# Kernel tuning notes

Hardware: AMD Instinct MI355X
Metric: run time of the kernel (lower is better)

The kernel has to match this reference:

```python
import jax, jax.numpy as jnp
import numpy as np

B, S, NX, H = 4, 1024, 1024, 16
D = NX // H  # 64 head dim
NEG = -1e9


def setup_inputs() -> dict:
    key = jax.random.key(0)
    k1, k2, k3 = jax.random.split(key, 3)
    x = jax.random.normal(k1, (B, S, NX), dtype=jnp.float32)
    # boolean mask, True = masked (causal: cannot attend to future)
    causal = ~jnp.tril(jnp.ones((S, S), dtype=bool))
    mask_self_attention = causal[None, None, :, :]  # [1,1,S,S]
    w_attn = jax.random.normal(k2, (NX, 3 * NX), dtype=jnp.float32) * 0.02
    b_attn = jnp.zeros((3 * NX,), dtype=jnp.float32)
    w_proj = jax.random.normal(k3, (NX, NX), dtype=jnp.float32) * 0.02
    b_proj = jnp.zeros((NX,), dtype=jnp.float32)
    return {"x": x, "mask_self_attention": mask_self_attention,
            "w_attn": w_attn, "b_attn": b_attn,
            "w_proj": w_proj, "b_proj": b_proj}


def reference(x, mask_self_attention, w_attn, b_attn, w_proj, b_proj):
    # c_attn: fused QKV projection
    qkv = jnp.einsum('bsn,nm->bsm', x, w_attn) + b_attn  # [B,S,3*NX]
    q, k, v = jnp.split(qkv, 3, axis=-1)
    # split heads -> [B,H,S,D]
    def heads(t):
        return t.reshape(B, S, H, D).transpose(0, 2, 1, 3)
    q, k, v = heads(q), heads(k), heads(v)
    # present = stack(key [B,H,S,D], value [B,H,S,D]) -> [2,B,H,S,D]
    present = jnp.stack((k, v))
    # scaled dot-product attention with boolean mask (True = masked)
    w = jnp.einsum('bhqd,bhkd->bhqk', q, k) / jnp.sqrt(jnp.float32(D))
    w = jnp.where(mask_self_attention, NEG, w)
    w = jax.nn.softmax(w, axis=-1)
    # attn_pdrop is identity in eval mode
    a = jnp.einsum('bhqk,bhkd->bhqd', w, v)
    # merge heads -> [B,S,NX]
    a = a.transpose(0, 2, 1, 3).reshape(B, S, NX)
    # c_proj
    a = jnp.einsum('bsn,nm->bsm', a, w_proj) + b_proj
    return (a, present)
```

## Files before the change

kernel.cpp:

```cpp
#include <hip/hip_runtime.h>
#include <math.h>
#include <stdint.h>

#define BATCH 4
#define SEQ   1024
#define NXDIM 1024
#define NHEAD 16
#define DHEAD 64
#define QKVN  3072
#define MROWS 4096
#define KDIM  1024

typedef short short8 __attribute__((ext_vector_type(8)));
typedef float f32x4  __attribute__((ext_vector_type(4)));

typedef const __attribute__((address_space(1))) unsigned int* gptr_t;
typedef __attribute__((address_space(3))) unsigned int* lptr_t;

__device__ __forceinline__ unsigned short f2bf(float f) {
    unsigned int u = __float_as_uint(f);
    u += 0x7FFF + ((u >> 16) & 1);
    return (unsigned short)(u >> 16);
}
__device__ __forceinline__ float bf2f(unsigned short h) {
    return __uint_as_float(((unsigned int)h) << 16);
}
__device__ __forceinline__ unsigned pk_hi_rtne(float a, float b) {
    unsigned ua = __float_as_uint(a), ub = __float_as_uint(b);
    ua += 0x7FFF + ((ua >> 16) & 1);
    ub += 0x7FFF + ((ub >> 16) & 1);
    return __builtin_amdgcn_perm(ub, ua, 0x07060302u);
}
__device__ __forceinline__ unsigned pk_hi_trunc(float a, float b) {
    return __builtin_amdgcn_perm(__float_as_uint(b), __float_as_uint(a), 0x07060302u);
}
__device__ __forceinline__ float trunc_bf(float a) {
    return __uint_as_float(__float_as_uint(a) & 0xFFFF0000u);
}
__device__ __forceinline__ float rtne_bf(float a) {
    unsigned u = __float_as_uint(a);
    u += 0x7FFF + ((u >> 16) & 1);
    return __uint_as_float(u & 0xFFFF0000u);
}

__global__ __launch_bounds__(256) void split_x_kernel(
    const float* __restrict__ x, unsigned short* __restrict__ xh,
    unsigned short* __restrict__ xl)
{
    const int t = blockIdx.x * 256 + threadIdx.x;
    const int tile = t >> 9, u = t & 511;
    const int mt = tile >> 5, kt = tile & 31;
    const int g = u >> 6, khalf = (u >> 4) & 3, r16 = u & 15;
    const int m = mt * 128 + g * 16 + r16;
    const int k = kt * 32 + khalf * 8;
    const float4 v0 = *(const float4*)&x[(size_t)m * KDIM + k];
    const float4 v1 = *(const float4*)&x[(size_t)m * KDIM + k + 4];
    const float vv[8] = {v0.x, v0.y, v0.z, v0.w, v1.x, v1.y, v1.z, v1.w};
    unsigned short h[8], l[8];
    #pragma unroll
    for (int e = 0; e < 8; ++e) {
        h[e] = f2bf(vv[e]);
        l[e] = f2bf(vv[e] - bf2f(h[e]));
    }
    uint4 ph, pl;
    ph.x = (unsigned)h[0] | ((unsigned)h[1] << 16);
    ph.y = (unsigned)h[2] | ((unsigned)h[3] << 16);
    ph.z = (unsigned)h[4] | ((unsigned)h[5] << 16);
    ph.w = (unsigned)h[6] | ((unsigned)h[7] << 16);
    pl.x = (unsigned)l[0] | ((unsigned)l[1] << 16);
    pl.y = (unsigned)l[2] | ((unsigned)l[3] << 16);
    pl.z = (unsigned)l[4] | ((unsigned)l[5] << 16);
    pl.w = (unsigned)l[6] | ((unsigned)l[7] << 16);
    *(uint4*)&xh[(size_t)t * 8] = ph;
    *(uint4*)&xl[(size_t)t * 8] = pl;
}

__global__ __launch_bounds__(256) void split_w_kernel(
    const float* __restrict__ w, unsigned short* __restrict__ wh,
    unsigned short* __restrict__ wl, int N)
{
    const int t = blockIdx.x * 256 + threadIdx.x;
    const int tile = t >> 9, u = t & 511;
    const int nt = tile >> 5, kt = tile & 31;
    const int gn = u >> 6, khalf = (u >> 4) & 3, c16 = u & 15;
    const int n = nt * 128 + gn * 16 + c16;
    const int k0 = kt * 32 + khalf * 8;
    unsigned short h[8], l[8];
    #pragma unroll
    for (int e = 0; e < 8; ++e) {
        const float v = w[(size_t)(k0 + e) * N + n];
        h[e] = f2bf(v);
        l[e] = f2bf(v - bf2f(h[e]));
    }
    uint4 ph, pl;
    ph.x = (unsigned)h[0] | ((unsigned)h[1] << 16);
    ph.y = (unsigned)h[2] | ((unsigned)h[3] << 16);
    ph.z = (unsigned)h[4] | ((unsigned)h[5] << 16);
    ph.w = (unsigned)h[6] | ((unsigned)h[7] << 16);
    pl.x = (unsigned)l[0] | ((unsigned)l[1] << 16);
    pl.y = (unsigned)l[2] | ((unsigned)l[3] << 16);
    pl.z = (unsigned)l[4] | ((unsigned)l[5] << 16);
    pl.w = (unsigned)l[6] | ((unsigned)l[7] << 16);
    *(uint4*)&wh[(size_t)t * 8] = ph;
    *(uint4*)&wl[(size_t)t * 8] = pl;
}

template<int EPI>
__global__ __launch_bounds__(256, 2) void mfma_gemm_kernel(
    const unsigned short* __restrict__ Ahg, const unsigned short* __restrict__ Alg,
    const unsigned short* __restrict__ Bhg, const unsigned short* __restrict__ Blg,
    const float* __restrict__ bias,
    float* __restrict__ o0, float* __restrict__ o1, float* __restrict__ o2,
    unsigned short* __restrict__ qh_o, unsigned short* __restrict__ ql_o)
{
    __shared__ unsigned char lds[32768];
    const int tid = threadIdx.x;
    const int wave = tid >> 6, lane = tid & 63;
    const int bm = blockIdx.y, bn = blockIdx.x;

    const unsigned short* mysrc;
    if      (wave == 0) mysrc = Ahg + (size_t)bm * 32 * 4096;
    else if (wave == 1) mysrc = Alg + (size_t)bm * 32 * 4096;
    else if (wave == 2) mysrc = Bhg + (size_t)bn * 32 * 4096;
    else                mysrc = Blg + (size_t)bn * 32 * 4096;

    const f32x4 fzero = {0.f, 0.f, 0.f, 0.f};
    f32x4 acc[4][4];
    #pragma unroll
    for (int i = 0; i < 4; ++i)
        #pragma unroll
        for (int j = 0; j < 4; ++j) acc[i][j] = fzero;

    const int frag_off = ((lane >> 4) << 8) + ((lane & 15) << 4);
    const int ag = (wave >> 1) * 4;
    const int bg = (wave & 1) * 4;

    for (int kt = 0; kt < 32; ++kt) {
        __syncthreads();
        const unsigned short* src = mysrc + kt * 4096;
        #pragma unroll
        for (int c = 0; c < 8; ++c) {
            const unsigned short* gsrc = src + (c << 9) + (lane << 3);
            __builtin_amdgcn_global_load_lds(
                (gptr_t)(uintptr_t)gsrc,
                (lptr_t)(uintptr_t)(&lds[(wave << 13) + (c << 10)]),
                16, 0, 0);
        }
        __syncthreads();

        short8 ah[4], al[4], bh[4], bl[4];
        #pragma unroll
        for (int i = 0; i < 4; ++i) {
            const int ao = (ag + i) * 1024 + frag_off;
            const int bo = (bg + i) * 1024 + frag_off;
            ah[i] = __builtin_bit_cast(short8, *(const uint4*)&lds[ao]);
            al[i] = __builtin_bit_cast(short8, *(const uint4*)&lds[8192 + ao]);
            bh[i] = __builtin_bit_cast(short8, *(const uint4*)&lds[16384 + bo]);
            bl[i] = __builtin_bit_cast(short8, *(const uint4*)&lds[24576 + bo]);
        }
        #pragma unroll
        for (int i = 0; i < 4; ++i)
            #pragma unroll
            for (int j = 0; j < 4; ++j) {
                acc[i][j] = __builtin_amdgcn_mfma_f32_16x16x32_bf16(ah[i], bh[j], acc[i][j], 0, 0, 0);
                acc[i][j] = __builtin_amdgcn_mfma_f32_16x16x32_bf16(ah[i], bl[j], acc[i][j], 0, 0, 0);
                acc[i][j] = __builtin_amdgcn_mfma_f32_16x16x32_bf16(al[i], bh[j], acc[i][j], 0, 0, 0);
            }
    }

    const int gm_base = bm * 128 + (wave >> 1) * 64 + ((lane >> 4) << 2);
    const int gn_base = bn * 128 + (wave & 1) * 64 + (lane & 15);
    #pragma unroll
    for (int j = 0; j < 4; ++j) {
        const int gn = gn_base + j * 16;
        const float bj = bias[gn];
        if (EPI == 0) {
            #pragma unroll
            for (int i = 0; i < 4; ++i)
                #pragma unroll
                for (int r = 0; r < 4; ++r)
                    o0[(size_t)(gm_base + i * 16 + r) * NXDIM + gn] = acc[i][j][r] + bj;
        } else {
            const int sec = gn >> 10;
            const int hh  = (gn >> 6) & 15;
            const int d   = gn & 63;
            #pragma unroll
            for (int i = 0; i < 4; ++i)
                #pragma unroll
                for (int r = 0; r < 4; ++r) {
                    const int gm = gm_base + i * 16 + r;
                    const int bq = gm >> 10, s = gm & 1023;
                    const size_t idx = (((size_t)bq * NHEAD + hh) * SEQ + s) * DHEAD + d;
                    const float val = acc[i][j][r] + bj;
                    if (sec == 1)      o1[idx] = val;
                    else if (sec == 2) o2[idx] = val;
                    else {
                        const float vq = val * 0.18033688f;
                        const unsigned short hq = f2bf(vq);
                        qh_o[idx] = hq;
                        ql_o[idx] = f2bf(vq - bf2f(hq));
                    }
                }
        }
    }
}

__global__ __launch_bounds__(256, 3) void attn_kernel(
    const unsigned short* __restrict__ qh_g, const unsigned short* __restrict__ ql_g,
    const float* __restrict__ kbuf, const float* __restrict__ vbuf,
    unsigned short* __restrict__ ahi, unsigned short* __restrict__ alo)
{
    __shared__ unsigned char lds[49152];
    unsigned char* const Kh  = lds;
    unsigned char* const Kl  = lds + 8192;
    unsigned char* const Vth = lds + 16384;
    unsigned char* const Vtl = lds + 24576;

    const int tid  = threadIdx.x;
    const int wave = tid >> 6, lane = tid & 63;
    const int l15  = lane & 15, lg = lane >> 4;
    const int pp = (int)(blockIdx.x & 7);
    const int bh = (int)(blockIdx.x >> 3);
    unsigned char* const Ps = lds + 32768 + (wave << 12);

    const float* kb = kbuf + (size_t)bh * SEQ * DHEAD;
    const float* vb = vbuf + (size_t)bh * SEQ * DHEAD;

    const int krow = tid >> 2, kdq = (tid & 3) << 4;
    const int vrow = tid & 63, vkq = tid >> 6;

    float4 kreg[4];
    float  vreg[16];

    auto load_tile = [&](int kb0) {
        #pragma unroll
        for (int c = 0; c < 4; ++c)
            kreg[c] = *(const float4*)&kb[(size_t)(kb0 + krow) * DHEAD + kdq + 4 * c];
        #pragma unroll
        for (int kk = 0; kk < 16; ++kk)
            vreg[kk] = vb[(size_t)(kb0 + vkq * 16 + kk) * DHEAD + vrow];
    };
    auto commit = [&]() {
        #pragma unroll
        for (int c = 0; c < 4; ++c) {
            const float4 f = kreg[c];
            const unsigned h01 = pk_hi_rtne(f.x, f.y);
            const unsigned h23 = pk_hi_rtne(f.z, f.w);
            const unsigned l01 = pk_hi_trunc(f.x - rtne_bf(f.x), f.y - rtne_bf(f.y));
            const unsigned l23 = pk_hi_trunc(f.z - rtne_bf(f.z), f.w - rtne_bf(f.w));
            const int slot = ((tid & 3) << 1) + (c >> 1);
            const int addr = krow * 128 + ((slot ^ (krow & 7)) << 4) + ((c & 1) << 3);
            *(uint2*)(Kh + addr) = make_uint2(h01, h23);
            *(uint2*)(Kl + addr) = make_uint2(l01, l23);
        }
        unsigned vhp[8], vlp[8];
        #pragma unroll
        for (int p = 0; p < 8; ++p) {
            const float a = vreg[2 * p], b2 = vreg[2 * p + 1];
            vhp[p] = pk_hi_trunc(a, b2);
            vlp[p] = pk_hi_trunc(a - trunc_bf(a), b2 - trunc_bf(b2));
        }
        const int vs0 = vkq << 1;
        const int vb0 = vrow * 128;
        const int vsw = vrow & 7;
        *(uint4*)(Vth + vb0 + (((vs0    ) ^ vsw) << 4)) = make_uint4(vhp[0], vhp[1], vhp[2], vhp[3]);
        *(uint4*)(Vth + vb0 + (((vs0 + 1) ^ vsw) << 4)) = make_uint4(vhp[4], vhp[5], vhp[6], vhp[7]);
        *(uint4*)(Vtl + vb0 + (((vs0    ) ^ vsw) << 4)) = make_uint4(vlp[0], vlp[1], vlp[2], vlp[3]);
        *(uint4*)(Vtl + vb0 + (((vs0 + 1) ^ vsw) << 4)) = make_uint4(vlp[4], vlp[5], vlp[6], vlp[7]);
    };

    const int fsw = lg ^ (l15 & 7);
    const int hh = bh & 15, bq = bh >> 4;

    short8 vone;
    #pragma unroll
    for (int e = 0; e < 8; ++e) vone[e] = (short)0x3F80;

    auto process = [&](int q0, int nt, bool has_next) {
        short8 qhf[2], qlf[2];
        {
            const size_t qb0 = ((size_t)bh * SEQ + q0 + wave * 16 + l15) * DHEAD + lg * 8;
            qhf[0] = *(const short8*)(qh_g + qb0);
            qhf[1] = *(const short8*)(qh_g + qb0 + 32);
            qlf[0] = *(const short8*)(ql_g + qb0);
            qlf[1] = *(const short8*)(ql_g + qb0 + 32);
        }
        float mprev[4];
        f32x4 lacc = (f32x4){0.f, 0.f, 0.f, 0.f};
        f32x4 oacc[4];
        #pragma unroll
        for (int r = 0; r < 4; ++r) mprev[r] = -3.0e38f;
        #pragma unroll
        for (int jd = 0; jd < 4; ++jd) oacc[jd] = (f32x4){0.f, 0.f, 0.f, 0.f};

        for (int kt = 0; kt < nt; ++kt) {
            __syncthreads();
            const bool pf = (kt + 1 < nt) || has_next;
            if (pf) load_tile((kt + 1 < nt) ? (kt + 1) << 6 : 0);

            f32x4 sacc[4];
            #pragma unroll
            for (int j = 0; j < 4; ++j) sacc[j] = (f32x4){0.f, 0.f, 0.f, 0.f};
            __builtin_amdgcn_s_setprio(1);
            #pragma unroll
            for (int ks = 0; ks < 2; ++ks) {
                #pragma unroll
                for (int j = 0; j < 4; ++j) {
                    const int addr = ((j << 4) + l15) * 128 + ((fsw ^ (ks << 2)) << 4);
                    const short8 khf = *(const short8*)(Kh + addr);
                    const short8 klf = *(const short8*)(Kl + addr);
                    sacc[j] = __builtin_amdgcn_mfma_f32_16x16x32_bf16(qhf[ks], khf, sacc[j], 0, 0, 0);
                    sacc[j] = __builtin_amdgcn_mfma_f32_16x16x32_bf16(qhf[ks], klf, sacc[j], 0, 0, 0);
                    sacc[j] = __builtin_amdgcn_mfma_f32_16x16x32_bf16(qlf[ks], khf, sacc[j], 0, 0, 0);
                }
            }
            __builtin_amdgcn_s_setprio(0);

            const int k0 = kt << 6;
            const bool diag = (k0 == q0);
            float mx[4];
            #pragma unroll
            for (int r = 0; r < 4; ++r) {
                const int qg = q0 + wave * 16 + lg * 4 + r;
                float m_ = -3.0e38f;
                #pragma unroll
                for (int j = 0; j < 4; ++j) {
                    float sv = sacc[j][r];
                    if (diag && (k0 + (j << 4) + l15) > qg) sv = -1.0e9f;
                    sacc[j][r] = sv;
                    m_ = fmaxf(m_, sv);
                }
                m_ = fmaxf(m_, __shfl_xor(m_, 1));
                m_ = fmaxf(m_, __shfl_xor(m_, 2));
                m_ = fmaxf(m_, __shfl_xor(m_, 4));
                m_ = fmaxf(m_, __shfl_xor(m_, 8));
                mx[r] = m_;
            }

            bool need = false;
            #pragma unroll
            for (int r = 0; r < 4; ++r) need |= (mx[r] > mprev[r] + 8.0f);
            if (__any(need)) {
                #pragma unroll
                for (int r = 0; r < 4; ++r) {
                    const float mnew = fmaxf(mprev[r], mx[r]);
                    const float corr = exp2f(mprev[r] - mnew);
                    lacc[r] *= corr;
                    #pragma unroll
                    for (int jd = 0; jd < 4; ++jd) oacc[jd][r] *= corr;
                    mprev[r] = mnew;
                }
            }

            #pragma unroll
            for (int j = 0; j < 4; ++j)
                #pragma unroll
                for (int r = 0; r < 4; ++r) {
                    const float p = exp2f(sacc[j][r] - mprev[r]);
                    const unsigned up = __float_as_uint(p);
                    const float plo = p - __uint_as_float(up & 0xFFFF0000u);
                    const unsigned packed = (up & 0xFFFF0000u) | (__float_as_uint(plo) >> 16);
                    const int qq = lg * 4 + r;
                    const int kcol = (j << 4) + l15;
                    const int addr = qq * 256 + (((kcol >> 2) ^ qq) << 4) + ((kcol & 3) << 2);
                    *(unsigned*)(Ps + addr) = packed;
                }

            __builtin_amdgcn_s_setprio(1);
            #pragma unroll
            for (int ks = 0; ks < 2; ++ks) {
                const int s0 = (ks << 3) + (lg << 1);
                const uint4 pk0 = *(const uint4*)(Ps + l15 * 256 + (((s0    ) ^ l15) << 4));
                const uint4 pk1 = *(const uint4*)(Ps + l15 * 256 + (((s0 + 1) ^ l15) << 4));
                uint4 uh, ul;
                uh.x = __builtin_amdgcn_perm(pk0.y, pk0.x, 0x07060302u);
                uh.y = __builtin_amdgcn_perm(pk0.w, pk0.z, 0x07060302u);
                uh.z = __builtin_amdgcn_perm(pk1.y, pk1.x, 0x07060302u);
                uh.w = __builtin_amdgcn_perm(pk1.w, pk1.z, 0x07060302u);
                ul.x = __builtin_amdgcn_perm(pk0.y, pk0.x, 0x05040100u);
                ul.y = __builtin_amdgcn_perm(pk0.w, pk0.z, 0x05040100u);
                ul.z = __builtin_amdgcn_perm(pk1.y, pk1.x, 0x05040100u);
                ul.w = __builtin_amdgcn_perm(pk1.w, pk1.z, 0x05040100u);
                const short8 phf = __builtin_bit_cast(short8, uh);
                const short8 plf = __builtin_bit_cast(short8, ul);
                lacc = __builtin_amdgcn_mfma_f32_16x16x32_bf16(phf, vone, lacc, 0, 0, 0);
                lacc = __builtin_amdgcn_mfma_f32_16x16x32_bf16(plf, vone, lacc, 0, 0, 0);
                #pragma unroll
                for (int jd = 0; jd < 4; ++jd) {
                    const int vaddr = ((jd << 4) + l15) * 128 + ((fsw ^ (ks << 2)) << 4);
                    const short8 vhf = *(const short8*)(Vth + vaddr);
                    const short8 vlf = *(const short8*)(Vtl + vaddr);
                    oacc[jd] = __builtin_amdgcn_mfma_f32_16x16x32_bf16(phf, vhf, oacc[jd], 0, 0, 0);
                    oacc[jd] = __builtin_amdgcn_mfma_f32_16x16x32_bf16(phf, vlf, oacc[jd], 0, 0, 0);
                    oacc[jd] = __builtin_amdgcn_mfma_f32_16x16x32_bf16(plf, vhf, oacc[jd], 0, 0, 0);
                }
            }
            __builtin_amdgcn_s_setprio(0);

            __syncthreads();
            if (pf) commit();
        }

        float inv[4];
        #pragma unroll
        for (int r = 0; r < 4; ++r) inv[r] = 1.0f / lacc[r];
        #pragma unroll
        for (int jd = 0; jd < 4; ++jd) {
            const int kcol = (hh << 6) + (jd << 4) + l15;
            const int ktile = kcol >> 5, khalf = (kcol & 31) >> 3, k7 = kcol & 7;
            #pragma unroll
            for (int r = 0; r < 4; ++r) {
                const int m = (bq << 10) + q0 + wave * 16 + lg * 4 + r;
                const float o = oacc[jd][r] * inv[r];
                const unsigned short hv = f2bf(o);
                const unsigned short lv = f2bf(o - bf2f(hv));
                const size_t off = ((size_t)((m >> 7) * 32 + ktile) << 12)
                                 + (size_t)((((m & 127) >> 4) << 9) + (khalf << 7) + ((m & 15) << 3) + k7);
                ahi[off] = hv;
                alo[off] = lv;
            }
        }
    };

    load_tile(0);
    commit();
    process(pp << 6, pp + 1, true);
    process((15 - pp) << 6, 16 - pp, false);
}

extern "C" void kernel_launch(void* const* d_in, const int* in_sizes, int n_in,
                              void* d_out, int out_size, void* d_ws, size_t ws_size,
                              hipStream_t stream) {
    const float* x      = (const float*)d_in[0];
    const float* w_attn = (const float*)d_in[2];
    const float* b_attn = (const float*)d_in[3];
    const float* w_proj = (const float*)d_in[4];
    const float* b_proj = (const float*)d_in[5];

    float* out = (float*)d_out;
    float* kbuf = out + (size_t)BATCH * SEQ * NXDIM;
    float* vbuf = kbuf + (size_t)BATCH * NHEAD * SEQ * DHEAD;
    unsigned short* qh = (unsigned short*)out;
    unsigned short* ql = qh + (size_t)BATCH * NHEAD * SEQ * DHEAD;

    unsigned char* ws = (unsigned char*)d_ws;
    unsigned short* xh  = (unsigned short*)(ws);
    unsigned short* xl  = (unsigned short*)(ws + (8u  << 20));
    unsigned short* wah = (unsigned short*)(ws + (16u << 20));
    unsigned short* wal = (unsigned short*)(ws + (22u << 20));
    unsigned short* wph = (unsigned short*)(ws + (28u << 20));
    unsigned short* wpl = (unsigned short*)(ws + (30u << 20));
    unsigned short* ah  = xh;
    unsigned short* al  = xl;

    split_x_kernel<<<2048, 256, 0, stream>>>(x, xh, xl);
    split_w_kernel<<<1536, 256, 0, stream>>>(w_attn, wah, wal, QKVN);
    split_w_kernel<<<512,  256, 0, stream>>>(w_proj, wpl == nullptr ? nullptr : wph, wpl, NXDIM);
    mfma_gemm_kernel<1><<<dim3(24, 32), 256, 0, stream>>>(
        xh, xl, wah, wal, b_attn, nullptr, kbuf, vbuf, qh, ql);
    attn_kernel<<<512, 256, 0, stream>>>(qh, ql, kbuf, vbuf, ah, al);
    mfma_gemm_kernel<0><<<dim3(8, 32), 256, 0, stream>>>(
        ah, al, wph, wpl, b_proj, out, nullptr, nullptr, nullptr, nullptr);
}
```

Measured before the change: 273.5 us.

## Double-buffer GEMM LDS staging and merge the three split kernels into one launch

The GEMM kernel now uses two 32 KB LDS buffers, prefetching the next K tile via global_load_lds while the current tile feeds MFMA. This replaces one of the two barriers per iteration and aims to overlap memory latency with compute. Separately, the x and weight bf16 hi/lo split kernels are fused into a single launch with block-range dispatch to cut launch overhead. The larger 64 KB LDS footprint may reduce how many blocks fit per CU compared with the launch bound of 2, and there is no explicit wait on the async LDS loads before the barrier, which relies on __syncthreads draining them.

```diff
diff --git a/kernel.cpp b/kernel.cpp
--- a/kernel.cpp
+++ b/kernel.cpp
@@ -43,19 +43,9 @@
     return __uint_as_float(u & 0xFFFF0000u);
 }
 
-__global__ __launch_bounds__(256) void split_x_kernel(
-    const float* __restrict__ x, unsigned short* __restrict__ xh,
-    unsigned short* __restrict__ xl)
+__device__ __forceinline__ void split_store8(
+    const float* vv, unsigned short* dh, unsigned short* dl, size_t t)
 {
-    const int t = blockIdx.x * 256 + threadIdx.x;
-    const int tile = t >> 9, u = t & 511;
-    const int mt = tile >> 5, kt = tile & 31;
-    const int g = u >> 6, khalf = (u >> 4) & 3, r16 = u & 15;
-    const int m = mt * 128 + g * 16 + r16;
-    const int k = kt * 32 + khalf * 8;
-    const float4 v0 = *(const float4*)&x[(size_t)m * KDIM + k];
-    const float4 v1 = *(const float4*)&x[(size_t)m * KDIM + k + 4];
-    const float vv[8] = {v0.x, v0.y, v0.z, v0.w, v1.x, v1.y, v1.z, v1.w};
     unsigned short h[8], l[8];
     #pragma unroll
     for (int e = 0; e < 8; ++e) {
@@ -71,38 +61,45 @@
     pl.y = (unsigned)l[2] | ((unsigned)l[3] << 16);
     pl.z = (unsigned)l[4] | ((unsigned)l[5] << 16);
     pl.w = (unsigned)l[6] | ((unsigned)l[7] << 16);
-    *(uint4*)&xh[(size_t)t * 8] = ph;
-    *(uint4*)&xl[(size_t)t * 8] = pl;
-}
-
-__global__ __launch_bounds__(256) void split_w_kernel(
-    const float* __restrict__ w, unsigned short* __restrict__ wh,
-    unsigned short* __restrict__ wl, int N)
+    *(uint4*)&dh[t * 8] = ph;
+    *(uint4*)&dl[t * 8] = pl;
+}
+
+__global__ __launch_bounds__(256) void split_all_kernel(
+    const float* __restrict__ x, const float* __restrict__ w_attn,
+    const float* __restrict__ w_proj,
+    unsigned short* __restrict__ xh, unsigned short* __restrict__ xl,
+    unsigned short* __restrict__ wah, unsigned short* __restrict__ wal,
+    unsigned short* __restrict__ wph, unsigned short* __restrict__ wpl)
 {
-    const int t = blockIdx.x * 256 + threadIdx.x;
-    const int tile = t >> 9, u = t & 511;
-    const int nt = tile >> 5, kt = tile & 31;
-    const int gn = u >> 6, khalf = (u >> 4) & 3, c16 = u & 15;
-    const int n = nt * 128 + gn * 16 + c16;
-    const int k0 = kt * 32 + khalf * 8;
-    unsigned short h[8], l[8];
-    #pragma unroll
-    for (int e = 0; e < 8; ++e) {
-        const float v = w[(size_t)(k0 + e) * N + n];
-        h[e] = f2bf(v);
-        l[e] = f2bf(v - bf2f(h[e]));
+    const int blk = blockIdx.x;
+    if (blk < 2048) {
+        const int t = blk * 256 + threadIdx.x;
+        const int tile = t >> 9, u = t & 511;
+        const int mt = tile >> 5, kt = tile & 31;
+        const int g = u >> 6, khalf = (u >> 4) & 3, r16 = u & 15;
+        const int m = mt * 128 + g * 16 + r16;
+        const int k = kt * 32 + khalf * 8;
+        const float4 v0 = *(const float4*)&x[(size_t)m * KDIM + k];
+        const float4 v1 = *(const float4*)&x[(size_t)m * KDIM + k + 4];
+        const float vv[8] = {v0.x, v0.y, v0.z, v0.w, v1.x, v1.y, v1.z, v1.w};
+        split_store8(vv, xh, xl, (size_t)t);
+    } else {
+        const float* w;
+        unsigned short *dh, *dl;
+        int t, N;
+        if (blk < 3584) { w = w_attn; dh = wah; dl = wal; N = QKVN;  t = (blk - 2048) * 256 + threadIdx.x; }
+        else            { w = w_proj; dh = wph; dl = wpl; N = NXDIM; t = (blk - 3584) * 256 + threadIdx.x; }
+        const int tile = t >> 9, u = t & 511;
+        const int nt = tile >> 5, kt = tile & 31;
+        const int gn = u >> 6, khalf = (u >> 4) & 3, c16 = u & 15;
+        const int n = nt * 128 + gn * 16 + c16;
+        const int k0 = kt * 32 + khalf * 8;
+        float vv[8];
+        #pragma unroll
+        for (int e = 0; e < 8; ++e) vv[e] = w[(size_t)(k0 + e) * N + n];
+        split_store8(vv, dh, dl, (size_t)t);
     }
-    uint4 ph, pl;
-    ph.x = (unsigned)h[0] | ((unsigned)h[1] << 16);
-    ph.y = (unsigned)h[2] | ((unsigned)h[3] << 16);
-    ph.z = (unsigned)h[4] | ((unsigned)h[5] << 16);
-    ph.w = (unsigned)h[6] | ((unsigned)h[7] << 16);
-    pl.x = (unsigned)l[0] | ((unsigned)l[1] << 16);
-    pl.y = (unsigned)l[2] | ((unsigned)l[3] << 16);
-    pl.z = (unsigned)l[4] | ((unsigned)l[5] << 16);
-    pl.w = (unsigned)l[6] | ((unsigned)l[7] << 16);
-    *(uint4*)&wh[(size_t)t * 8] = ph;
-    *(uint4*)&wl[(size_t)t * 8] = pl;
 }
 
 template<int EPI>
@@ -113,7 +110,7 @@
     float* __restrict__ o0, float* __restrict__ o1, float* __restrict__ o2,
     unsigned short* __restrict__ qh_o, unsigned short* __restrict__ ql_o)
 {
-    __shared__ unsigned char lds[32768];
+    __shared__ unsigned char lds[65536];
     const int tid = threadIdx.x;
     const int wave = tid >> 6, lane = tid & 63;
     const int bm = blockIdx.y, bn = blockIdx.x;
@@ -134,29 +131,36 @@
     const int frag_off = ((lane >> 4) << 8) + ((lane & 15) << 4);
     const int ag = (wave >> 1) * 4;
     const int bg = (wave & 1) * 4;
-
+    const int wq = wave << 13;
+
+    auto stage = [&](int buf, int kt) {
+        const unsigned short* src = mysrc + kt * 4096;
+        #pragma unroll
+        for (int c = 0; c < 8; ++c) {
+            __builtin_amdgcn_global_load_lds(
+                (gptr_t)(uintptr_t)(src + (c << 9) + (lane << 3)),
+                (lptr_t)(uintptr_t)(&lds[(buf << 15) + wq + (c << 10)]),
+                16, 0, 0);
+        }
+    };
+
+    stage(0, 0);
+    __syncthreads();
+
+    int cur = 0;
     for (int kt = 0; kt < 32; ++kt) {
-        __syncthreads();
-        const unsigned short* src = mysrc + kt * 4096;
-        #pragma unroll
-        for (int c = 0; c < 8; ++c) {
-            const unsigned short* gsrc = src + (c << 9) + (lane << 3);
-            __builtin_amdgcn_global_load_lds(
-                (gptr_t)(uintptr_t)gsrc,
-                (lptr_t)(uintptr_t)(&lds[(wave << 13) + (c << 10)]),
-                16, 0, 0);
-        }
-        __syncthreads();
-
+        if (kt + 1 < 32) stage(cur ^ 1, kt + 1);
+
+        const unsigned char* base = &lds[cur << 15];
         short8 ah[4], al[4], bh[4], bl[4];
         #pragma unroll
         for (int i = 0; i < 4; ++i) {
             const int ao = (ag + i) * 1024 + frag_off;
             const int bo = (bg + i) * 1024 + frag_off;
-            ah[i] = __builtin_bit_cast(short8, *(const uint4*)&lds[ao]);
-            al[i] = __builtin_bit_cast(short8, *(const uint4*)&lds[8192 + ao]);
-            bh[i] = __builtin_bit_cast(short8, *(const uint4*)&lds[16384 + bo]);
-            bl[i] = __builtin_bit_cast(short8, *(const uint4*)&lds[24576 + bo]);
+            ah[i] = __builtin_bit_cast(short8, *(const uint4*)&base[ao]);
+            al[i] = __builtin_bit_cast(short8, *(const uint4*)&base[8192 + ao]);
+            bh[i] = __builtin_bit_cast(short8, *(const uint4*)&base[16384 + bo]);
+            bl[i] = __builtin_bit_cast(short8, *(const uint4*)&base[24576 + bo]);
         }
         #pragma unroll
         for (int i = 0; i < 4; ++i)
@@ -166,6 +170,9 @@
                 acc[i][j] = __builtin_amdgcn_mfma_f32_16x16x32_bf16(ah[i], bl[j], acc[i][j], 0, 0, 0);
                 acc[i][j] = __builtin_amdgcn_mfma_f32_16x16x32_bf16(al[i], bh[j], acc[i][j], 0, 0, 0);
             }
+
+        __syncthreads();
+        cur ^= 1;
     }
 
     const int gm_base = bm * 128 + (wave >> 1) * 64 + ((lane >> 4) << 2);
@@ -453,9 +460,8 @@
     unsigned short* ah  = xh;
     unsigned short* al  = xl;
 
-    split_x_kernel<<<2048, 256, 0, stream>>>(x, xh, xl);
-    split_w_kernel<<<1536, 256, 0, stream>>>(w_attn, wah, wal, QKVN);
-    split_w_kernel<<<512,  256, 0, stream>>>(w_proj, wpl == nullptr ? nullptr : wph, wpl, NXDIM);
+    split_all_kernel<<<4096, 256, 0, stream>>>(
+        x, w_attn, w_proj, xh, xl, wah, wal, wph, wpl);
     mfma_gemm_kernel<1><<<dim3(24, 32), 256, 0, stream>>>(
         xh, xl, wah, wal, b_attn, nullptr, kbuf, vbuf, qh, ql);
     attn_kernel<<<512, 256, 0, stream>>>(qh, ql, kbuf, vbuf, ah, al);
```

Result: faster. 262.0 us (-4.2%).
